# Optimization experiments

Hardware: AMD Instinct MI355X
Metric: run time of the kernel (lower is better)

The kernel has to match this reference:

```python
import jax, jax.numpy as jnp
import numpy as np

N = 4096

def setup_inputs() -> dict:
    key = jax.random.key(0)
    kA, kB = jax.random.split(key)
    # A and B are upper-triangular inputs, as the module assumes
    A = jnp.triu(jax.random.normal(kA, (N, N), dtype=jnp.float32))
    B = jnp.triu(jax.random.normal(kB, (N, N), dtype=jnp.float32))
    return {"A": A, "B": B}

def reference(A, B):
    # C = triu(A @ B); product of upper-triangular matrices is upper-triangular,
    # the kernel additionally masks the lower triangle of the output.
    return jnp.triu(A @ B)
```

## Files before the change

### kernel.cpp

```cpp
#include <hip/hip_runtime.h>


#define N   4096
#define NB  32
#define BM  128
#define BK  32
#define CH  8
#define NWG 1000

typedef __attribute__((ext_vector_type(8))) __bf16 bf16x8;
typedef __attribute__((ext_vector_type(4))) float  floatx4;
typedef __attribute__((ext_vector_type(8))) unsigned short ushort8;

typedef const __attribute__((address_space(1))) void* gas_ptr;
typedef __attribute__((address_space(3))) void*       las_ptr;

__device__ __forceinline__ unsigned short f32_to_bf16_rne(float f) {
    unsigned u = __builtin_bit_cast(unsigned, f);
    unsigned r = u + 0x7fffu + ((u >> 16) & 1u);
    return (unsigned short)(r >> 16);
}

__global__ void conv_a_kernel(const float* __restrict__ A,
                              unsigned short* __restrict__ Ab) {
    const int bid = blockIdx.x;
    const int row = bid >> 2;
    const int k0  = (bid & 3) * 1024;
    const int rb  = row >> 7;
    if (((k0 >> 7) + 8) <= rb) return;
    const int idx = row * N + k0 + threadIdx.x * 4;
    const float4 v = *(const float4*)(A + idx);
    ushort4 o;
    o.x = f32_to_bf16_rne(v.x);
    o.y = f32_to_bf16_rne(v.y);
    o.z = f32_to_bf16_rne(v.z);
    o.w = f32_to_bf16_rne(v.w);
    *(ushort4*)(Ab + idx) = o;
}

__global__ void conv_bt_kernel(const float* __restrict__ B,
                               unsigned short* __restrict__ Bt) {
    __shared__ float tile[64][65];
    const int jb = blockIdx.x;
    const int kb = blockIdx.y;
    if ((kb >> 1) > (jb >> 1)) return;
    const int j0 = jb * 64, k0 = kb * 64;
    const int t  = threadIdx.x;
    {
        const int kl = t >> 2;
        const int j4 = (t & 3) * 16;
        const float* src = B + (size_t)(k0 + kl) * N + j0 + j4;
        const float4 v0 = ((const float4*)src)[0];
        const float4 v1 = ((const float4*)src)[1];
        const float4 v2 = ((const float4*)src)[2];
        const float4 v3 = ((const float4*)src)[3];
        float* dst = &tile[kl][j4];
        dst[0]=v0.x; dst[1]=v0.y; dst[2]=v0.z; dst[3]=v0.w;
        dst[4]=v1.x; dst[5]=v1.y; dst[6]=v1.z; dst[7]=v1.w;
        dst[8]=v2.x; dst[9]=v2.y; dst[10]=v2.z; dst[11]=v2.w;
        dst[12]=v3.x; dst[13]=v3.y; dst[14]=v3.z; dst[15]=v3.w;
    }
    __syncthreads();
    {
        const int jl = t >> 2;
        const int k4 = (t & 3) * 16;
        ushort8 o0, o1;
        #pragma unroll
        for (int i = 0; i < 8; ++i) o0[i] = f32_to_bf16_rne(tile[k4 + i][jl]);
        #pragma unroll
        for (int i = 0; i < 8; ++i) o1[i] = f32_to_bf16_rne(tile[k4 + 8 + i][jl]);
        unsigned short* dst = Bt + (size_t)(j0 + jl) * N + k0 + k4;
        ((ushort8*)dst)[0] = o0;
        ((ushort8*)dst)[1] = o1;
    }
}

__global__ __launch_bounds__(256)
void trimm_kernel(const unsigned short* __restrict__ Ab,
                  const unsigned short* __restrict__ Bt,
                  float* __restrict__ C) {
    __shared__ unsigned short sA[2][BM * BK];
    __shared__ unsigned short sB[2][BM * BK];

    int rem = blockIdx.x;
    int d = 0, per = 1;
    for (int dd = NB - 1; dd >= 0; --dd) {
        const int p   = (dd + CH) / CH;
        const int cnt = (NB - dd) * p;
        if (rem < cnt) { d = dd; per = p; break; }
        rem -= cnt;
    }
    const int tile  = rem / per;
    const int chunk = rem - tile * per;
    const int bi = tile, bj = tile + d;
    const int c    = d + 1;
    const int base = c / per, extra = c - base * per;
    const int kb0  = bi + chunk * base + (chunk < extra ? chunk : extra);
    const int len  = base + (chunk < extra ? 1 : 0);

    const int tid  = threadIdx.x;
    const int w    = tid >> 6;
    const int lane = tid & 63;
    const int quad = lane >> 4;
    const int l15  = lane & 15;

    const int m0 = (w >> 1) * 64;
    const int n0 = (w & 1) * 64;
    const int row0 = bi * BM;
    const int col0 = bj * BM;

    floatx4 acc[4][4] = {};

    const int srow = lane >> 2;
    const int skk  = (lane & 3) * 8;
    const int q0 = w * 2, q1 = w * 2 + 1;
    const int r0 = q0 * 16 + srow, r1 = q1 * 16 + srow;

    const unsigned short* gA0 = Ab + (size_t)(row0 + r0) * N + kb0 * BM + skk;
    const unsigned short* gA1 = Ab + (size_t)(row0 + r1) * N + kb0 * BM + skk;
    const unsigned short* gB0 = Bt + (size_t)(col0 + r0) * N + kb0 * BM + skk;
    const unsigned short* gB1 = Bt + (size_t)(col0 + r1) * N + kb0 * BM + skk;

    const int ns2 = len * 2;
    for (int s2 = 0; s2 < ns2; ++s2) {
        __builtin_amdgcn_global_load_lds((gas_ptr)gA0, (las_ptr)&sA[0][q0 * 512], 16, 0, 0);
        __builtin_amdgcn_global_load_lds((gas_ptr)gA1, (las_ptr)&sA[0][q1 * 512], 16, 0, 0);
        __builtin_amdgcn_global_load_lds((gas_ptr)gB0, (las_ptr)&sB[0][q0 * 512], 16, 0, 0);
        __builtin_amdgcn_global_load_lds((gas_ptr)gB1, (las_ptr)&sB[0][q1 * 512], 16, 0, 0);
        __builtin_amdgcn_global_load_lds((gas_ptr)(gA0 + BK), (las_ptr)&sA[1][q0 * 512], 16, 0, 0);
        __builtin_amdgcn_global_load_lds((gas_ptr)(gA1 + BK), (las_ptr)&sA[1][q1 * 512], 16, 0, 0);
        __builtin_amdgcn_global_load_lds((gas_ptr)(gB0 + BK), (las_ptr)&sB[1][q0 * 512], 16, 0, 0);
        __builtin_amdgcn_global_load_lds((gas_ptr)(gB1 + BK), (las_ptr)&sB[1][q1 * 512], 16, 0, 0);
        gA0 += 2 * BK; gA1 += 2 * BK; gB0 += 2 * BK; gB1 += 2 * BK;
        __syncthreads();

        #pragma unroll
        for (int h = 0; h < 2; ++h) {
            bf16x8 af[4], bfr[4];
            #pragma unroll
            for (int t = 0; t < 4; ++t) {
                af[t]  = *(const bf16x8*)&sA[h][(m0 + t * 16 + l15) * BK + quad * 8];
                bfr[t] = *(const bf16x8*)&sB[h][(n0 + t * 16 + l15) * BK + quad * 8];
            }
            #pragma unroll
            for (int tm = 0; tm < 4; ++tm)
                #pragma unroll
                for (int tn = 0; tn < 4; ++tn)
                    acc[tm][tn] = __builtin_amdgcn_mfma_f32_16x16x32_bf16(
                        af[tm], bfr[tn], acc[tm][tn], 0, 0, 0);
        }
        __syncthreads();
    }

    #pragma unroll
    for (int tm = 0; tm < 4; ++tm) {
        const int grow_base = row0 + m0 + tm * 16 + quad * 4;
        #pragma unroll
        for (int tn = 0; tn < 4; ++tn) {
            const int gcol = col0 + n0 + tn * 16 + l15;
            #pragma unroll
            for (int r = 0; r < 4; ++r) {
                const int grow = grow_base + r;
                float* p = C + (size_t)grow * N + gcol;
                const float v = acc[tm][tn][r];
                if (per > 1) {
                    atomicAdd(p, v);
                } else if (d != 0) {
                    *p = v;
                } else if (gcol >= grow) {
                    *p = v;
                }
            }
        }
    }
}

extern "C" void kernel_launch(void* const* d_in, const int* in_sizes, int n_in,
                              void* d_out, int out_size, void* d_ws, size_t ws_size,
                              hipStream_t stream) {
    const float* A = (const float*)d_in[0];
    const float* B = (const float*)d_in[1];
    float* C = (float*)d_out;

    unsigned short* Ab = (unsigned short*)d_ws;
    unsigned short* Bt = Ab + (size_t)N * N;

    hipMemsetAsync(d_out, 0, (size_t)N * N * sizeof(float), stream);
    conv_a_kernel<<<dim3(N * 4), dim3(256), 0, stream>>>(A, Ab);
    conv_bt_kernel<<<dim3(N / 64, N / 64), dim3(256), 0, stream>>>(B, Bt);
    trimm_kernel<<<dim3(NWG), dim3(256), 0, stream>>>(Ab, Bt, C);
}
```

Measured before the change: 243.8 us.

## Fuse prep kernels with selective output zeroing and register-prefetch the GEMM loop

The two conversion kernels and the full-output memset are merged into one prep kernel. It converts A, transposes and converts B, and zeroes only the C tiles that are never plainly stored: the lower triangle and the split-K atomic tiles. Diagonal tiles now write explicit zeros below the diagonal. The GEMM main loop drops direct global-to-LDS loads with two barriers per step and instead prefetches into registers and double-buffers LDS with one barrier per BK step. This cuts output write traffic and launch count, but the register staging adds VGPR pressure and may change latency hiding.

Result: no change. 243.0 us (-0.3%).

```diff
diff --git a/kernel.cpp b/kernel.cpp
--- a/kernel.cpp
+++ b/kernel.cpp
@@ -12,66 +12,68 @@
 typedef __attribute__((ext_vector_type(4))) float  floatx4;
 typedef __attribute__((ext_vector_type(8))) unsigned short ushort8;
 
-typedef const __attribute__((address_space(1))) void* gas_ptr;
-typedef __attribute__((address_space(3))) void*       las_ptr;
-
 __device__ __forceinline__ unsigned short f32_to_bf16_rne(float f) {
     unsigned u = __builtin_bit_cast(unsigned, f);
     unsigned r = u + 0x7fffu + ((u >> 16) & 1u);
     return (unsigned short)(r >> 16);
 }
 
-__global__ void conv_a_kernel(const float* __restrict__ A,
-                              unsigned short* __restrict__ Ab) {
-    const int bid = blockIdx.x;
-    const int row = bid >> 2;
-    const int k0  = (bid & 3) * 1024;
-    const int rb  = row >> 7;
-    if (((k0 >> 7) + 8) <= rb) return;
-    const int idx = row * N + k0 + threadIdx.x * 4;
-    const float4 v = *(const float4*)(A + idx);
-    ushort4 o;
-    o.x = f32_to_bf16_rne(v.x);
-    o.y = f32_to_bf16_rne(v.y);
-    o.z = f32_to_bf16_rne(v.z);
-    o.w = f32_to_bf16_rne(v.w);
-    *(ushort4*)(Ab + idx) = o;
-}
+__global__ __launch_bounds__(256)
+void prep_kernel(const float* __restrict__ A, const float* __restrict__ B,
+                 unsigned short* __restrict__ Ab, unsigned short* __restrict__ Bt,
+                 float* __restrict__ C) {
+    __shared__ float tile[64][65];
+    const int bx = blockIdx.x, by = blockIdx.y;
+    const int x0 = bx * 64, y0 = by * 64;
+    const int xb = bx >> 1, yb = by >> 1;
+    const int t  = threadIdx.x;
+    const int tr = t >> 2, tc = (t & 3) * 16;
 
-__global__ void conv_bt_kernel(const float* __restrict__ B,
-                               unsigned short* __restrict__ Bt) {
-    __shared__ float tile[64][65];
-    const int jb = blockIdx.x;
-    const int kb = blockIdx.y;
-    if ((kb >> 1) > (jb >> 1)) return;
-    const int j0 = jb * 64, k0 = kb * 64;
-    const int t  = threadIdx.x;
-    {
-        const int kl = t >> 2;
-        const int j4 = (t & 3) * 16;
-        const float* src = B + (size_t)(k0 + kl) * N + j0 + j4;
+    if (xb >= yb) {
+        const float* src = A + (size_t)(y0 + tr) * N + x0 + tc;
         const float4 v0 = ((const float4*)src)[0];
         const float4 v1 = ((const float4*)src)[1];
         const float4 v2 = ((const float4*)src)[2];
         const float4 v3 = ((const float4*)src)[3];
-        float* dst = &tile[kl][j4];
-        dst[0]=v0.x; dst[1]=v0.y; dst[2]=v0.z; dst[3]=v0.w;
-        dst[4]=v1.x; dst[5]=v1.y; dst[6]=v1.z; dst[7]=v1.w;
-        dst[8]=v2.x; dst[9]=v2.y; dst[10]=v2.z; dst[11]=v2.w;
-        dst[12]=v3.x; dst[13]=v3.y; dst[14]=v3.z; dst[15]=v3.w;
+        ushort8 o0, o1;
+        o0[0]=f32_to_bf16_rne(v0.x); o0[1]=f32_to_bf16_rne(v0.y);
+        o0[2]=f32_to_bf16_rne(v0.z); o0[3]=f32_to_bf16_rne(v0.w);
+        o0[4]=f32_to_bf16_rne(v1.x); o0[5]=f32_to_bf16_rne(v1.y);
+        o0[6]=f32_to_bf16_rne(v1.z); o0[7]=f32_to_bf16_rne(v1.w);
+        o1[0]=f32_to_bf16_rne(v2.x); o1[1]=f32_to_bf16_rne(v2.y);
+        o1[2]=f32_to_bf16_rne(v2.z); o1[3]=f32_to_bf16_rne(v2.w);
+        o1[4]=f32_to_bf16_rne(v3.x); o1[5]=f32_to_bf16_rne(v3.y);
+        o1[6]=f32_to_bf16_rne(v3.z); o1[7]=f32_to_bf16_rne(v3.w);
+        unsigned short* dst = Ab + (size_t)(y0 + tr) * N + x0 + tc;
+        ((ushort8*)dst)[0] = o0;
+        ((ushort8*)dst)[1] = o1;
     }
-    __syncthreads();
-    {
-        const int jl = t >> 2;
-        const int k4 = (t & 3) * 16;
+    if (xb <= yb) {
+        const float* src = B + (size_t)(x0 + tr) * N + y0 + tc;
+        const float4 v0 = ((const float4*)src)[0];
+        const float4 v1 = ((const float4*)src)[1];
+        const float4 v2 = ((const float4*)src)[2];
+        const float4 v3 = ((const float4*)src)[3];
+        float* d = &tile[tr][tc];
+        d[0]=v0.x; d[1]=v0.y; d[2]=v0.z; d[3]=v0.w;
+        d[4]=v1.x; d[5]=v1.y; d[6]=v1.z; d[7]=v1.w;
+        d[8]=v2.x; d[9]=v2.y; d[10]=v2.z; d[11]=v2.w;
+        d[12]=v3.x; d[13]=v3.y; d[14]=v3.z; d[15]=v3.w;
+        __syncthreads();
         ushort8 o0, o1;
         #pragma unroll
-        for (int i = 0; i < 8; ++i) o0[i] = f32_to_bf16_rne(tile[k4 + i][jl]);
+        for (int i = 0; i < 8; ++i) o0[i] = f32_to_bf16_rne(tile[tc + i][tr]);
         #pragma unroll
-        for (int i = 0; i < 8; ++i) o1[i] = f32_to_bf16_rne(tile[k4 + 8 + i][jl]);
-        unsigned short* dst = Bt + (size_t)(j0 + jl) * N + k0 + k4;
+        for (int i = 0; i < 8; ++i) o1[i] = f32_to_bf16_rne(tile[tc + 8 + i][tr]);
+        unsigned short* dst = Bt + (size_t)(y0 + tr) * N + x0 + tc;
         ((ushort8*)dst)[0] = o0;
         ((ushort8*)dst)[1] = o1;
+    }
+    if (xb < yb || (xb - yb) >= CH) {
+        float4 z = {0.f, 0.f, 0.f, 0.f};
+        float* dst = C + (size_t)(y0 + tr) * N + x0 + tc;
+        ((float4*)dst)[0] = z; ((float4*)dst)[1] = z;
+        ((float4*)dst)[2] = z; ((float4*)dst)[3] = z;
     }
 }
 
@@ -115,41 +117,46 @@
     const int skk  = (lane & 3) * 8;
     const int q0 = w * 2, q1 = w * 2 + 1;
     const int r0 = q0 * 16 + srow, r1 = q1 * 16 + srow;
+    const int lofs0 = q0 * 512 + srow * 32 + skk;
+    const int lofs1 = q1 * 512 + srow * 32 + skk;
 
     const unsigned short* gA0 = Ab + (size_t)(row0 + r0) * N + kb0 * BM + skk;
     const unsigned short* gA1 = Ab + (size_t)(row0 + r1) * N + kb0 * BM + skk;
     const unsigned short* gB0 = Bt + (size_t)(col0 + r0) * N + kb0 * BM + skk;
     const unsigned short* gB1 = Bt + (size_t)(col0 + r1) * N + kb0 * BM + skk;
 
-    const int ns2 = len * 2;
-    for (int s2 = 0; s2 < ns2; ++s2) {
-        __builtin_amdgcn_global_load_lds((gas_ptr)gA0, (las_ptr)&sA[0][q0 * 512], 16, 0, 0);
-        __builtin_amdgcn_global_load_lds((gas_ptr)gA1, (las_ptr)&sA[0][q1 * 512], 16, 0, 0);
-        __builtin_amdgcn_global_load_lds((gas_ptr)gB0, (las_ptr)&sB[0][q0 * 512], 16, 0, 0);
-        __builtin_amdgcn_global_load_lds((gas_ptr)gB1, (las_ptr)&sB[0][q1 * 512], 16, 0, 0);
-        __builtin_amdgcn_global_load_lds((gas_ptr)(gA0 + BK), (las_ptr)&sA[1][q0 * 512], 16, 0, 0);
-        __builtin_amdgcn_global_load_lds((gas_ptr)(gA1 + BK), (las_ptr)&sA[1][q1 * 512], 16, 0, 0);
-        __builtin_amdgcn_global_load_lds((gas_ptr)(gB0 + BK), (las_ptr)&sB[1][q0 * 512], 16, 0, 0);
-        __builtin_amdgcn_global_load_lds((gas_ptr)(gB1 + BK), (las_ptr)&sB[1][q1 * 512], 16, 0, 0);
-        gA0 += 2 * BK; gA1 += 2 * BK; gB0 += 2 * BK; gB1 += 2 * BK;
+    const int ns = len * 4;
+
+    ushort8 aR0 = *(const ushort8*)gA0;  gA0 += BK;
+    ushort8 aR1 = *(const ushort8*)gA1;  gA1 += BK;
+    ushort8 bR0 = *(const ushort8*)gB0;  gB0 += BK;
+    ushort8 bR1 = *(const ushort8*)gB1;  gB1 += BK;
+
+    for (int s = 0; s < ns; ++s) {
+        const int buf = s & 1;
+        *(ushort8*)&sA[buf][lofs0] = aR0;
+        *(ushort8*)&sA[buf][lofs1] = aR1;
+        *(ushort8*)&sB[buf][lofs0] = bR0;
+        *(ushort8*)&sB[buf][lofs1] = bR1;
         __syncthreads();
-
+        if (s + 1 < ns) {
+            aR0 = *(const ushort8*)gA0;  gA0 += BK;
+            aR1 = *(const ushort8*)gA1;  gA1 += BK;
+            bR0 = *(const ushort8*)gB0;  gB0 += BK;
+            bR1 = *(const ushort8*)gB1;  gB1 += BK;
+        }
+        bf16x8 af[4], bfr[4];
         #pragma unroll
-        for (int h = 0; h < 2; ++h) {
-            bf16x8 af[4], bfr[4];
+        for (int t = 0; t < 4; ++t) {
+            af[t]  = *(const bf16x8*)&sA[buf][(m0 + t * 16 + l15) * BK + quad * 8];
+            bfr[t] = *(const bf16x8*)&sB[buf][(n0 + t * 16 + l15) * BK + quad * 8];
+        }
+        #pragma unroll
+        for (int tm = 0; tm < 4; ++tm)
             #pragma unroll
-            for (int t = 0; t < 4; ++t) {
-                af[t]  = *(const bf16x8*)&sA[h][(m0 + t * 16 + l15) * BK + quad * 8];
-                bfr[t] = *(const bf16x8*)&sB[h][(n0 + t * 16 + l15) * BK + quad * 8];
-            }
-            #pragma unroll
-            for (int tm = 0; tm < 4; ++tm)
-                #pragma unroll
-                for (int tn = 0; tn < 4; ++tn)
-                    acc[tm][tn] = __builtin_amdgcn_mfma_f32_16x16x32_bf16(
-                        af[tm], bfr[tn], acc[tm][tn], 0, 0, 0);
-        }
-        __syncthreads();
+            for (int tn = 0; tn < 4; ++tn)
+                acc[tm][tn] = __builtin_amdgcn_mfma_f32_16x16x32_bf16(
+                    af[tm], bfr[tn], acc[tm][tn], 0, 0, 0);
     }
 
     #pragma unroll
@@ -167,8 +174,8 @@
                     atomicAdd(p, v);
                 } else if (d != 0) {
                     *p = v;
-                } else if (gcol >= grow) {
-                    *p = v;
+                } else {
+                    *p = (gcol >= grow) ? v : 0.0f;
                 }
             }
         }
@@ -185,8 +192,6 @@
     unsigned short* Ab = (unsigned short*)d_ws;
     unsigned short* Bt = Ab + (size_t)N * N;
 
-    hipMemsetAsync(d_out, 0, (size_t)N * N * sizeof(float), stream);
-    conv_a_kernel<<<dim3(N * 4), dim3(256), 0, stream>>>(A, Ab);
-    conv_bt_kernel<<<dim3(N / 64, N / 64), dim3(256), 0, stream>>>(B, Bt);
+    prep_kernel<<<dim3(N / 64, N / 64), dim3(256), 0, stream>>>(A, B, Ab, Bt, C);
     trimm_kernel<<<dim3(NWG), dim3(256), 0, stream>>>(Ab, Bt, C);
 }
```
